# Performance work log

Measured on AMD Instinct MI355X. Metric: run time of the kernel, lower is better.

The kernel has to match this reference:

```python
import jax, jax.numpy as jnp
import numpy as np

B, DIM, T, H, MAX_T = 8, 512, 4096, 64, 4096


def setup_inputs() -> dict:
    key = jax.random.key(0)
    ks = jax.random.split(key, 10)
    s = 0.02  # small init scale keeps exp() well-conditioned, like xavier init
    x = jax.random.normal(ks[0], (B, DIM, T), dtype=jnp.float32)
    wq = jax.random.normal(ks[1], (H, DIM), dtype=jnp.float32) * s
    bq = jnp.zeros((H,), dtype=jnp.float32)
    wk = jax.random.normal(ks[2], (H, DIM), dtype=jnp.float32) * s
    bk = jnp.zeros((H,), dtype=jnp.float32)
    wv = jax.random.normal(ks[3], (H, DIM), dtype=jnp.float32) * s
    bv = jnp.zeros((H,), dtype=jnp.float32)
    wp = jax.random.normal(ks[4], (DIM, H), dtype=jnp.float32) * s
    bp = jnp.zeros((DIM,), dtype=jnp.float32)
    # xavier_uniform on [MAX_T, MAX_T]: bound = sqrt(6/(MAX_T+MAX_T))
    bound = float(np.sqrt(6.0 / (MAX_T + MAX_T)))
    wbias = jax.random.uniform(ks[5], (MAX_T, MAX_T), dtype=jnp.float32,
                               minval=-bound, maxval=bound)
    return {"x": x, "wq": wq, "bq": bq, "wk": wk, "bk": bk,
            "wv": wv, "bv": bv, "wp": wp, "bp": bp, "wbias": wbias}


def reference(x, wq, bq, wk, bk, wv, bv, wp, bp, wbias):
    # x: [B, dim, T] -> [B, T, dim]
    xt = jnp.swapaxes(x, 1, 2)
    t = xt.shape[1]
    Q = xt @ wq.T + bq            # [B, T, H]
    K = xt @ wk.T + bk            # [B, T, H]
    V = xt @ wv.T + bv            # [B, T, H]
    ew = jnp.exp(wbias[:t, :t])   # [T, T]
    eK = jnp.exp(K)               # [B, T, H]
    num = jnp.einsum('ts,bsh->bth', ew, eK * V)  # exp(w) @ (exp(K)*V)
    den = jnp.einsum('ts,bsh->bth', ew, eK)      # exp(w) @ exp(K)
    Yt = jax.nn.sigmoid(Q) * (num / den)          # [B, T, H]
    out = Yt @ wp.T + bp                          # [B, T, dim]
    return (out, out)
```

## Files before the change

### kernel.cpp

```cpp
#include <hip/hip_runtime.h>
#include <hip/hip_bf16.h>

#define B_   8
#define DIM_ 512
#define T_   4096
#define H_   64
#define NC_  1024

typedef __attribute__((ext_vector_type(8))) short short8;
typedef __attribute__((ext_vector_type(4))) float f32x4;

__device__ __forceinline__ unsigned short f2bf(float x) {
    __hip_bfloat16 h = __float2bfloat16(x);
    return *reinterpret_cast<unsigned short*>(&h);
}
__device__ __forceinline__ float bf2f(unsigned short u) {
    __hip_bfloat16 h = *reinterpret_cast<__hip_bfloat16*>(&u);
    return __bfloat162float(h);
}
__device__ __forceinline__ void gload16(const void* g, void* l) {
    __builtin_amdgcn_global_load_lds(
        (const __attribute__((address_space(1))) unsigned int*)g,
        (__attribute__((address_space(3))) unsigned int*)l, 16, 0, 0);
}

__global__ __launch_bounds__(256) void ewb_kernel(
    const float* __restrict__ wb, unsigned short* __restrict__ Aexp)
{
    const int n4 = T_ * T_ / 4;
    int idx = blockIdx.x * blockDim.x + threadIdx.x;
    int stride = gridDim.x * blockDim.x;
    for (int i = idx; i < n4; i += stride) {
        float4 v = ((const float4*)wb)[i];
        ushort4 o;
        o.x = f2bf(__expf(v.x));
        o.y = f2bf(__expf(v.y));
        o.z = f2bf(__expf(v.z));
        o.w = f2bf(__expf(v.w));
        ((ushort4*)Aexp)[i] = o;
    }
}

__global__ __launch_bounds__(128) void wcat_kernel(
    const float* __restrict__ wq, const float* __restrict__ bq,
    const float* __restrict__ wk, const float* __restrict__ bk,
    const float* __restrict__ wv, const float* __restrict__ bv,
    unsigned short* __restrict__ Wcat, float* __restrict__ bcat)
{
    const int r = blockIdx.x;
    const int tid = threadIdx.x;
    const float* src = (r < 64) ? (wq + (size_t)r * DIM_)
                     : (r < 128) ? (wk + (size_t)(r - 64) * DIM_)
                                 : (wv + (size_t)(r - 128) * DIM_);
    const int d4 = tid * 4;
    float4 v = *(const float4*)&src[d4];
    ushort4 o;
    o.x = f2bf(v.x); o.y = f2bf(v.y); o.z = f2bf(v.z); o.w = f2bf(v.w);
    *(ushort4*)&Wcat[(size_t)r * DIM_ + d4] = o;
    if (tid == 0)
        bcat[r] = (r < 64) ? bq[r] : (r < 128) ? bk[r - 64] : bv[r - 128];
}

__global__ __launch_bounds__(256) void wpb_kernel(
    const float* __restrict__ wp, unsigned short* __restrict__ wpb)
{
    const int i = (blockIdx.x * 256 + threadIdx.x) * 4;
    float4 v = *(const float4*)&wp[i];
    ushort4 o;
    o.x = f2bf(v.x); o.y = f2bf(v.y); o.z = f2bf(v.z); o.w = f2bf(v.w);
    *(ushort4*)&wpb[i] = o;
}

__global__ __launch_bounds__(256) void xqkv_fused(
    const float* __restrict__ x, const unsigned short* __restrict__ Wcat,
    const float* __restrict__ bcat,
    unsigned short* __restrict__ Qb, unsigned short* __restrict__ SbT)
{
    __shared__ float xs[64 * 65];
    __shared__ unsigned short Bs[192 * 64];

    const int tid = threadIdx.x;
    const int t0 = blockIdx.x * 64;
    const int b  = blockIdx.y;
    const int wid = tid >> 6, lane = tid & 63;

    f32x4 acc[12];
    const f32x4 vzero = {0.f, 0.f, 0.f, 0.f};
#pragma unroll
    for (int f = 0; f < 12; f++) acc[f] = vzero;

    const int rs  = tid >> 3;
    const int ks8 = (tid & 7) * 8;
    const unsigned short* Bg = Wcat + (size_t)rs * DIM_ + ks8;

    const int xrow = tid >> 4;
    const int xt4  = (tid & 15) * 4;

    const int t_in = lane & 15;
    const int g    = lane >> 4;

    for (int d0 = 0; d0 < DIM_; d0 += 64) {
#pragma unroll
        for (int p = 0; p < 4; p++) {
            const int d = p * 16 + xrow;
            float4 v = *(const float4*)&x[((size_t)b * DIM_ + d0 + d) * T_ + t0 + xt4];
            *(float4*)&xs[d * 65 + xt4] = v;
        }
#pragma unroll
        for (int it = 0; it < 6; it++)
            gload16(Bg + (size_t)(it * 32) * DIM_ + d0, (void*)&Bs[(it * 256 + tid) * 8]);
        __syncthreads();

        const int row_a = wid * 16 + t_in;
#pragma unroll
        for (int kk = 0; kk < 2; kk++) {
            union { unsigned short s[8]; short8 v; } af;
#pragma unroll
            for (int j = 0; j < 8; j++)
                af.s[j] = f2bf(xs[(kk * 32 + g * 8 + j) * 65 + row_a]);
            const int kr = kk * 32 + g * 8;
#pragma unroll
            for (int fn = 0; fn < 12; fn++) {
                short8 bf = *(const short8*)&Bs[(fn * 16 + t_in) * 64 + kr];
                acc[fn] = __builtin_amdgcn_mfma_f32_16x16x32_bf16(af.v, bf, acc[fn], 0, 0, 0);
            }
        }
        __syncthreads();
    }

    const int cc = t_in;
    const int t_base = t0 + wid * 16 + g * 4;

#pragma unroll
    for (int fn = 0; fn < 4; fn++) {
        const int h = fn * 16 + cc;
        const float bb = bcat[h];
#pragma unroll
        for (int r = 0; r < 4; r++)
            Qb[((size_t)b * T_ + t_base + r) * H_ + h] = f2bf(acc[fn][r] + bb);
    }
#pragma unroll
    for (int f = 0; f < 4; f++) {
        const int h = f * 16 + cc;
        const float bK = bcat[64 + h];
        const float bV = bcat[128 + h];
        ushort4 pk, pe;
        float e0 = __expf(acc[4 + f][0] + bK), v0 = acc[8 + f][0] + bV;
        float e1 = __expf(acc[4 + f][1] + bK), v1 = acc[8 + f][1] + bV;
        float e2 = __expf(acc[4 + f][2] + bK), v2 = acc[8 + f][2] + bV;
        float e3 = __expf(acc[4 + f][3] + bK), v3 = acc[8 + f][3] + bV;
        pe.x = f2bf(e0); pe.y = f2bf(e1); pe.z = f2bf(e2); pe.w = f2bf(e3);
        pk.x = f2bf(e0 * v0); pk.y = f2bf(e1 * v1); pk.z = f2bf(e2 * v2); pk.w = f2bf(e3 * v3);
        *(ushort4*)&SbT[(size_t)(b * 64 + h) * T_ + t_base] = pk;
        *(ushort4*)&SbT[(size_t)(512 + b * 64 + h) * T_ + t_base] = pe;
    }
}

__global__ __launch_bounds__(256) void aft_gemm_mfma(
    const unsigned short* __restrict__ Aexp,
    const unsigned short* __restrict__ SbT,
    unsigned short* __restrict__ ND)
{
    __shared__ unsigned short As[128 * 64];
    __shared__ unsigned short Bs[128 * 64];

    const int tid = threadIdx.x;
    const int lin = blockIdx.x + (blockIdx.y << 3) + (blockIdx.z << 8);
    const int swz = ((lin & 7) << 6) + (lin >> 3);
    const int c0 = (swz & 7) * 128;
    const int t0 = ((swz >> 3) & 31) * 128;
    const int ks = swz >> 8;
    const int sbase = ks * (T_ / 2);

    const int wid = tid >> 6, lane = tid & 63;
    const int wm = wid >> 1, wn = wid & 1;

    f32x4 acc[4][4];
    const f32x4 vzero = {0.f, 0.f, 0.f, 0.f};
#pragma unroll
    for (int a = 0; a < 4; a++)
#pragma unroll
        for (int b2 = 0; b2 < 4; b2++) acc[a][b2] = vzero;

    const int rs  = tid >> 3;
    const int ks8 = (tid & 7) * 8;
    const unsigned short* Ag = Aexp + (size_t)(t0 + rs) * T_ + sbase + ks8;
    const unsigned short* Bg = SbT  + (size_t)(c0 + rs) * T_ + sbase + ks8;

    for (int s0 = 0; s0 < T_ / 2; s0 += 64) {
#pragma unroll
        for (int it = 0; it < 4; it++) {
            gload16(Ag + (size_t)(it * 32) * T_ + s0, (void*)&As[(it * 256 + tid) * 8]);
            gload16(Bg + (size_t)(it * 32) * T_ + s0, (void*)&Bs[(it * 256 + tid) * 8]);
        }
        __syncthreads();
        const int row_a = wm * 64 + (lane & 15);
        const int row_b = wn * 64 + (lane & 15);
#pragma unroll
        for (int kk = 0; kk < 2; kk++) {
            const int kr = kk * 32 + (lane >> 4) * 8;
            short8 af[4], bfr[4];
#pragma unroll
            for (int f = 0; f < 4; f++)
                af[f] = *(const short8*)&As[(row_a + f * 16) * 64 + kr];
#pragma unroll
            for (int f = 0; f < 4; f++)
                bfr[f] = *(const short8*)&Bs[(row_b + f * 16) * 64 + kr];
#pragma unroll
            for (int fm = 0; fm < 4; fm++)
#pragma unroll
                for (int fn = 0; fn < 4; fn++)
                    acc[fm][fn] = __builtin_amdgcn_mfma_f32_16x16x32_bf16(
                        af[fm], bfr[fn], acc[fm][fn], 0, 0, 0);
        }
        __syncthreads();
    }

    unsigned short* NDp = ND + (size_t)ks * T_ * NC_;
    const int r4 = (lane >> 4) * 4;
    const int cc = lane & 15;
#pragma unroll
    for (int fm = 0; fm < 4; fm++)
#pragma unroll
        for (int fn = 0; fn < 4; fn++)
#pragma unroll
            for (int r = 0; r < 4; r++) {
                const int t = t0 + wm * 64 + fm * 16 + r4 + r;
                const int c = c0 + wn * 64 + fn * 16 + cc;
                NDp[(size_t)t * NC_ + c] = f2bf(acc[fm][fn][r]);
            }
}

__global__ __launch_bounds__(256) void epilogue_mfma(
    const unsigned short* __restrict__ Qb, const unsigned short* __restrict__ ND,
    const unsigned short* __restrict__ wpb, const float* __restrict__ bp,
    float* __restrict__ out, int write_both)
{
    __shared__ unsigned short smem[36864];
    unsigned short* y_s  = smem;
    unsigned short* wp_s = smem + 4096;
    float* st = (float*)smem;

    const int tid  = threadIdx.x;
    const int t0   = blockIdx.x * 64;
    const int b    = blockIdx.y;
    const int wid  = tid >> 6, lane = tid & 63;
    const size_t SZ_COPY = (size_t)B_ * T_ * DIM_;

    {
        const int rs = tid >> 3;
        const int c8 = tid & 7;
#pragma unroll
        for (int p = 0; p < 16; p++) {
            const int row = p * 32 + rs;
            gload16(wpb + (size_t)row * 64 + ((c8 ^ (row & 7)) << 3),
                    (void*)&wp_s[((size_t)row * 8 + c8) * 8]);
        }
    }
    {
        const int t   = tid >> 2;
        const int h16 = (tid & 3) * 16;
        const unsigned short* ND1 = ND + (size_t)T_ * NC_;
        const size_t qoff = ((size_t)b * T_ + t0 + t) * H_ + h16;
        const size_t noff = (size_t)(t0 + t) * NC_ + b * 64 + h16;
        float yv[16];
#pragma unroll
        for (int u = 0; u < 16; u++) {
            float q   = bf2f(Qb[qoff + u]);
            float num = bf2f(ND[noff + u]) + bf2f(ND1[noff + u]);
            float den = bf2f(ND[noff + 512 + u]) + bf2f(ND1[noff + 512 + u]);
            yv[u] = (1.f / (1.f + __expf(-q))) * num / den;
        }
#pragma unroll
        for (int u = 0; u < 2; u++) {
            const int h8 = (tid & 3) * 2 + u;
            union { unsigned short s[8]; short8 v; } pk;
#pragma unroll
            for (int e = 0; e < 8; e++) pk.s[e] = f2bf(yv[u * 8 + e]);
            *(short8*)((char*)y_s + t * 128 + ((h8 ^ (t & 7)) << 4)) = pk.v;
        }
    }
    __syncthreads();

    f32x4 acc[32];
    const f32x4 vzero = {0.f, 0.f, 0.f, 0.f};
#pragma unroll
    for (int f = 0; f < 32; f++) acc[f] = vzero;

    const int ra = wid * 16 + (lane & 15);
    short8 af[2];
#pragma unroll
    for (int kk = 0; kk < 2; kk++)
        af[kk] = *(const short8*)((char*)y_s + ra * 128 +
                                  (((kk * 4 + (lane >> 4)) ^ (ra & 7)) << 4));
#pragma unroll
    for (int fn = 0; fn < 32; fn++) {
        const int rb = fn * 16 + (lane & 15);
#pragma unroll
        for (int kk = 0; kk < 2; kk++) {
            short8 bf = *(const short8*)((char*)wp_s + rb * 128 +
                                         (((kk * 4 + (lane >> 4)) ^ (rb & 7)) << 4));
            acc[fn] = __builtin_amdgcn_mfma_f32_16x16x32_bf16(af[kk], bf, acc[fn], 0, 0, 0);
        }
    }
    __syncthreads();

    const int g  = lane >> 4;
    const int cc = lane & 15;
    float4 bb01[2];
    bb01[0] = *(const float4*)&bp[lane * 4];
    bb01[1] = *(const float4*)&bp[256 + lane * 4];

#pragma unroll
    for (int ch = 0; ch < 2; ch++) {
        if (ch) __syncthreads();
#pragma unroll
        for (int f = 0; f < 16; f++)
#pragma unroll
            for (int r = 0; r < 4; r++)
                st[(wid * 16 + g * 4 + r) * 260 + f * 16 + cc] = acc[ch * 16 + f][r];
        __syncthreads();
        const float4 bb = bb01[ch];
#pragma unroll
        for (int it = 0; it < 16; it++) {
            const int row = it * 4 + wid;
            float4 v = *(const float4*)&st[row * 260 + lane * 4];
            float4 o = {v.x + bb.x, v.y + bb.y, v.z + bb.z, v.w + bb.w};
            const size_t obase = ((size_t)b * T_ + t0 + row) * DIM_ + ch * 256 + lane * 4;
            *(float4*)&out[obase] = o;
            if (write_both)
                *(float4*)&out[SZ_COPY + obase] = o;
        }
    }
}

__global__ void dup_kernel(const float4* __restrict__ src, float4* __restrict__ dst, int n4)
{
    int idx = blockIdx.x * blockDim.x + threadIdx.x;
    int stride = gridDim.x * blockDim.x;
    for (int k = idx; k < n4; k += stride) dst[k] = src[k];
}

extern "C" void kernel_launch(void* const* d_in, const int* in_sizes, int n_in,
                              void* d_out, int out_size, void* d_ws, size_t ws_size,
                              hipStream_t stream)
{
    const float* x     = (const float*)d_in[0];
    const float* wq    = (const float*)d_in[1];
    const float* bq    = (const float*)d_in[2];
    const float* wk    = (const float*)d_in[3];
    const float* bk    = (const float*)d_in[4];
    const float* wv    = (const float*)d_in[5];
    const float* bv    = (const float*)d_in[6];
    const float* wp    = (const float*)d_in[7];
    const float* bp    = (const float*)d_in[8];
    const float* wbias = (const float*)d_in[9];
    float* out = (float*)d_out;

    const size_t SZ_COPY = (size_t)B_ * T_ * DIM_;

    const size_t NEED = 63177472;
    char* R;
    int write_both;
    if (ws_size >= NEED) {
        R = (char*)d_ws;
        write_both = 1;
    } else {
        R = (char*)(out + SZ_COPY);
        write_both = 0;
    }
    unsigned short* Aexp  = (unsigned short*)R;
    unsigned short* NDbuf = (unsigned short*)(R + 33554432);
    unsigned short* SbT   = (unsigned short*)(R + 50331648);
    unsigned short* Qbuf  = (unsigned short*)(R + 58720256);
    unsigned short* Wcat  = (unsigned short*)(R + 62914560);
    unsigned short* wpb   = (unsigned short*)(R + 63111168);
    float*          bcat  = (float*)(R + 63176704);

    ewb_kernel<<<2048, 256, 0, stream>>>(wbias, Aexp);
    wcat_kernel<<<192, 128, 0, stream>>>(wq, bq, wk, bk, wv, bv, Wcat, bcat);
    wpb_kernel<<<32, 256, 0, stream>>>(wp, wpb);
    xqkv_fused<<<dim3(T_ / 64, B_), 256, 0, stream>>>(x, Wcat, bcat, Qbuf, SbT);
    aft_gemm_mfma<<<dim3(NC_ / 128, T_ / 128, 2), 256, 0, stream>>>(Aexp, SbT, NDbuf);
    epilogue_mfma<<<dim3(T_ / 64, B_), 256, 0, stream>>>(Qbuf, NDbuf, wpb, bp, out, write_both);
    if (!write_both)
        dup_kernel<<<2048, 256, 0, stream>>>((const float4*)out,
                                             (float4*)(out + SZ_COPY),
                                             (int)(SZ_COPY / 4));
}
```

Measured before the change: 149.9 us.

## Rewrite AFT GEMM with 256x256 tiles, 8-phase double-buffered pipeline and split-K 4

Replaces the 128x128 single-buffered GEMM with a 512-thread, 256x256-tile kernel that double-buffers LDS and interleaves global-to-LDS loads across four MFMA phases per K step. It uses XOR-swizzled LDS layout and setprio around the MFMA bursts. The split-K factor rises to 4 when workspace allows, with the epilogue summing a variable number of partials. The aim is to hide load latency and raise arithmetic intensity, at the cost of more partial-sum traffic and 128KB of LDS per block.

```diff
diff --git a/kernel.cpp b/kernel.cpp
--- a/kernel.cpp
+++ b/kernel.cpp
@@ -156,77 +156,139 @@
     }
 }
 
-__global__ __launch_bounds__(256) void aft_gemm_mfma(
+__global__ __launch_bounds__(512, 2) void aft_gemm_8ph(
     const unsigned short* __restrict__ Aexp,
     const unsigned short* __restrict__ SbT,
-    unsigned short* __restrict__ ND)
-{
-    __shared__ unsigned short As[128 * 64];
-    __shared__ unsigned short Bs[128 * 64];
-
-    const int tid = threadIdx.x;
-    const int lin = blockIdx.x + (blockIdx.y << 3) + (blockIdx.z << 8);
-    const int swz = ((lin & 7) << 6) + (lin >> 3);
-    const int c0 = (swz & 7) * 128;
-    const int t0 = ((swz >> 3) & 31) * 128;
-    const int ks = swz >> 8;
-    const int sbase = ks * (T_ / 2);
-
-    const int wid = tid >> 6, lane = tid & 63;
-    const int wm = wid >> 1, wn = wid & 1;
-
-    f32x4 acc[4][4];
+    unsigned short* __restrict__ ND, int SK)
+{
+    __shared__ unsigned short smem[65536];
+
+    const int tid  = threadIdx.x;
+    const int wid  = tid >> 6, lane = tid & 63;
+    const int wm   = wid >> 2, wn = wid & 3;
+    const int la   = lane & 15, lg = lane >> 4;
+
+    const int nwg = 64 * SK;
+    const int lin = blockIdx.x + blockIdx.y * 4 + blockIdx.z * 64;
+    const int cpx = nwg >> 3;
+    const int wg  = (lin & 7) * cpx + (lin >> 3);
+    const int c0  = (wg & 3) * 256;
+    const int t0  = ((wg >> 2) & 15) * 256;
+    const int ks  = wg >> 6;
+    const int Kblk  = T_ / SK;
+    const int sbase = ks * Kblk;
+    const int NT    = Kblk >> 6;
+
+    f32x4 acc[8][4];
     const f32x4 vzero = {0.f, 0.f, 0.f, 0.f};
 #pragma unroll
-    for (int a = 0; a < 4; a++)
-#pragma unroll
-        for (int b2 = 0; b2 < 4; b2++) acc[a][b2] = vzero;
-
-    const int rs  = tid >> 3;
-    const int ks8 = (tid & 7) * 8;
-    const unsigned short* Ag = Aexp + (size_t)(t0 + rs) * T_ + sbase + ks8;
-    const unsigned short* Bg = SbT  + (size_t)(c0 + rs) * T_ + sbase + ks8;
-
-    for (int s0 = 0; s0 < T_ / 2; s0 += 64) {
-#pragma unroll
-        for (int it = 0; it < 4; it++) {
-            gload16(Ag + (size_t)(it * 32) * T_ + s0, (void*)&As[(it * 256 + tid) * 8]);
-            gload16(Bg + (size_t)(it * 32) * T_ + s0, (void*)&Bs[(it * 256 + tid) * 8]);
-        }
-        __syncthreads();
-        const int row_a = wm * 64 + (lane & 15);
-        const int row_b = wn * 64 + (lane & 15);
-#pragma unroll
-        for (int kk = 0; kk < 2; kk++) {
-            const int kr = kk * 32 + (lane >> 4) * 8;
-            short8 af[4], bfr[4];
-#pragma unroll
-            for (int f = 0; f < 4; f++)
-                af[f] = *(const short8*)&As[(row_a + f * 16) * 64 + kr];
-#pragma unroll
-            for (int f = 0; f < 4; f++)
-                bfr[f] = *(const short8*)&Bs[(row_b + f * 16) * 64 + kr];
-#pragma unroll
-            for (int fm = 0; fm < 4; fm++)
-#pragma unroll
-                for (int fn = 0; fn < 4; fn++)
-                    acc[fm][fn] = __builtin_amdgcn_mfma_f32_16x16x32_bf16(
-                        af[fm], bfr[fn], acc[fm][fn], 0, 0, 0);
-        }
-        __syncthreads();
+    for (int i = 0; i < 8; i++)
+#pragma unroll
+        for (int j = 0; j < 4; j++) acc[i][j] = vzero;
+
+    const int lr8 = tid >> 3, c16 = tid & 7;
+
+    auto stA = [&](int q, int T, int p) {
+        const int tr = (lr8 < 32) ? (32 * q + lr8) : (96 + 32 * q + lr8);
+        const unsigned short* src = Aexp + (size_t)(t0 + tr) * T_
+                                  + sbase + T * 64 + ((c16 ^ (tr & 7)) * 8);
+        gload16(src, (void*)&smem[p * 32768 + tr * 64 + c16 * 8]);
+    };
+    auto stB = [&](int h, int j, int T, int p) {
+        const int tr = 128 * h + 64 * j + lr8;
+        const unsigned short* src = SbT + (size_t)(c0 + tr) * T_
+                                  + sbase + T * 64 + ((c16 ^ (tr & 7)) * 8);
+        gload16(src, (void*)&smem[p * 32768 + 16384 + tr * 64 + c16 * 8]);
+    };
+
+    stB(0, 0, 0, 0); stB(0, 1, 0, 0); stB(1, 0, 0, 0); stB(1, 1, 0, 0);
+    stA(0, 0, 0);    stA(1, 0, 0);    stA(2, 0, 0);    stA(3, 0, 0);
+    stB(0, 0, 1, 1); stB(0, 1, 1, 1); stB(1, 0, 1, 1); stB(1, 1, 1, 1);
+    stA(0, 1, 1);    stA(1, 1, 1);
+    asm volatile("s_waitcnt vmcnt(6)" ::: "memory");
+    __builtin_amdgcn_s_barrier();
+
+    for (int kt = 0; kt < NT; ++kt) {
+        const int p = kt & 1;
+        const unsigned short* Ab = smem + p * 32768;
+        const unsigned short* Bb = Ab + 16384;
+        short8 bfr[4][2];
+
+        {
+            short8 af[2][2];
+#pragma unroll
+            for (int i = 0; i < 2; ++i) {
+                const int row = 128 * wm + 16 * i + la;
+#pragma unroll
+                for (int kk = 0; kk < 2; ++kk)
+                    af[i][kk] = *(const short8*)&Ab[row * 64 + (((kk * 4 + lg) ^ (row & 7)) * 8)];
+            }
+#pragma unroll
+            for (int fn = 0; fn < 4; ++fn) {
+                const int row = 64 * wn + 16 * fn + la;
+#pragma unroll
+                for (int kk = 0; kk < 2; ++kk)
+                    bfr[fn][kk] = *(const short8*)&Bb[row * 64 + (((kk * 4 + lg) ^ (row & 7)) * 8)];
+            }
+            if (kt + 1 < NT) { stA(2, kt + 1, 1 - p); stA(3, kt + 1, 1 - p); }
+            __builtin_amdgcn_s_barrier();
+            asm volatile("s_waitcnt lgkmcnt(0)" ::: "memory");
+            __builtin_amdgcn_sched_barrier(0);
+            __builtin_amdgcn_s_setprio(1);
+#pragma unroll
+            for (int i = 0; i < 2; ++i)
+#pragma unroll
+                for (int fn = 0; fn < 4; ++fn)
+#pragma unroll
+                    for (int kk = 0; kk < 2; ++kk)
+                        acc[i][fn] = __builtin_amdgcn_mfma_f32_16x16x32_bf16(
+                            af[i][kk], bfr[fn][kk], acc[i][fn], 0, 0, 0);
+            __builtin_amdgcn_s_setprio(0);
+            __builtin_amdgcn_s_barrier();
+        }
+#pragma unroll
+        for (int q = 1; q < 4; ++q) {
+            short8 af[2][2];
+#pragma unroll
+            for (int i = 0; i < 2; ++i) {
+                const int row = 128 * wm + 16 * (2 * q + i) + la;
+#pragma unroll
+                for (int kk = 0; kk < 2; ++kk)
+                    af[i][kk] = *(const short8*)&Ab[row * 64 + (((kk * 4 + lg) ^ (row & 7)) * 8)];
+            }
+            if (kt + 2 < NT) {
+                if (q == 1)      { stB(0, 0, kt + 2, p); stB(0, 1, kt + 2, p); }
+                else if (q == 2) { stB(1, 0, kt + 2, p); stB(1, 1, kt + 2, p); }
+                else             { stA(0, kt + 2, p);    stA(1, kt + 2, p);    }
+            }
+            if (q == 3) asm volatile("s_waitcnt vmcnt(6)" ::: "memory");
+            __builtin_amdgcn_s_barrier();
+            asm volatile("s_waitcnt lgkmcnt(0)" ::: "memory");
+            __builtin_amdgcn_sched_barrier(0);
+            __builtin_amdgcn_s_setprio(1);
+#pragma unroll
+            for (int i = 0; i < 2; ++i)
+#pragma unroll
+                for (int fn = 0; fn < 4; ++fn)
+#pragma unroll
+                    for (int kk = 0; kk < 2; ++kk)
+                        acc[2 * q + i][fn] = __builtin_amdgcn_mfma_f32_16x16x32_bf16(
+                            af[i][kk], bfr[fn][kk], acc[2 * q + i][fn], 0, 0, 0);
+            __builtin_amdgcn_s_setprio(0);
+            __builtin_amdgcn_s_barrier();
+        }
     }
 
     unsigned short* NDp = ND + (size_t)ks * T_ * NC_;
-    const int r4 = (lane >> 4) * 4;
-    const int cc = lane & 15;
-#pragma unroll
-    for (int fm = 0; fm < 4; fm++)
-#pragma unroll
-        for (int fn = 0; fn < 4; fn++)
-#pragma unroll
-            for (int r = 0; r < 4; r++) {
-                const int t = t0 + wm * 64 + fm * 16 + r4 + r;
-                const int c = c0 + wn * 64 + fn * 16 + cc;
+    const int r4 = lg * 4;
+#pragma unroll
+    for (int fm = 0; fm < 8; ++fm)
+#pragma unroll
+        for (int fn = 0; fn < 4; ++fn)
+#pragma unroll
+            for (int r = 0; r < 4; ++r) {
+                const int t = t0 + 128 * wm + 16 * fm + r4 + r;
+                const int c = c0 + 64 * wn + 16 * fn + la;
                 NDp[(size_t)t * NC_ + c] = f2bf(acc[fm][fn][r]);
             }
 }
@@ -234,7 +296,7 @@
 __global__ __launch_bounds__(256) void epilogue_mfma(
     const unsigned short* __restrict__ Qb, const unsigned short* __restrict__ ND,
     const unsigned short* __restrict__ wpb, const float* __restrict__ bp,
-    float* __restrict__ out, int write_both)
+    float* __restrict__ out, int write_both, int SK)
 {
     __shared__ unsigned short smem[36864];
     unsigned short* y_s  = smem;
@@ -260,15 +322,18 @@
     {
         const int t   = tid >> 2;
         const int h16 = (tid & 3) * 16;
-        const unsigned short* ND1 = ND + (size_t)T_ * NC_;
         const size_t qoff = ((size_t)b * T_ + t0 + t) * H_ + h16;
         const size_t noff = (size_t)(t0 + t) * NC_ + b * 64 + h16;
         float yv[16];
 #pragma unroll
         for (int u = 0; u < 16; u++) {
-            float q   = bf2f(Qb[qoff + u]);
-            float num = bf2f(ND[noff + u]) + bf2f(ND1[noff + u]);
-            float den = bf2f(ND[noff + 512 + u]) + bf2f(ND1[noff + 512 + u]);
+            float num = 0.f, den = 0.f;
+            for (int pp = 0; pp < SK; ++pp) {
+                const unsigned short* NDp = ND + (size_t)pp * T_ * NC_;
+                num += bf2f(NDp[noff + u]);
+                den += bf2f(NDp[noff + 512 + u]);
+            }
+            float q = bf2f(Qb[qoff + u]);
             yv[u] = (1.f / (1.f + __expf(-q))) * num / den;
         }
 #pragma unroll
@@ -359,30 +424,33 @@
 
     const size_t SZ_COPY = (size_t)B_ * T_ * DIM_;
 
-    const size_t NEED = 63177472;
+    auto need = [](int SK) -> size_t {
+        return 33554432u + (size_t)SK * 8388608u + 8388608u + 4194304u
+             + 196608u + 65536u + 1024u;
+    };
+    int SK, write_both;
     char* R;
-    int write_both;
-    if (ws_size >= NEED) {
-        R = (char*)d_ws;
-        write_both = 1;
+    if (ws_size >= need(4)) {
+        SK = 4; write_both = 1; R = (char*)d_ws;
     } else {
-        R = (char*)(out + SZ_COPY);
-        write_both = 0;
-    }
-    unsigned short* Aexp  = (unsigned short*)R;
-    unsigned short* NDbuf = (unsigned short*)(R + 33554432);
-    unsigned short* SbT   = (unsigned short*)(R + 50331648);
-    unsigned short* Qbuf  = (unsigned short*)(R + 58720256);
-    unsigned short* Wcat  = (unsigned short*)(R + 62914560);
-    unsigned short* wpb   = (unsigned short*)(R + 63111168);
-    float*          bcat  = (float*)(R + 63176704);
+        SK = 2; write_both = 0; R = (char*)(out + SZ_COPY);
+    }
+    size_t off = 0;
+    unsigned short* Aexp  = (unsigned short*)(R + off); off += 33554432u;
+    unsigned short* NDbuf = (unsigned short*)(R + off); off += (size_t)SK * 8388608u;
+    unsigned short* SbT   = (unsigned short*)(R + off); off += 8388608u;
+    unsigned short* Qbuf  = (unsigned short*)(R + off); off += 4194304u;
+    unsigned short* Wcat  = (unsigned short*)(R + off); off += 196608u;
+    unsigned short* wpb   = (unsigned short*)(R + off); off += 65536u;
+    float*          bcat  = (float*)(R + off);
 
     ewb_kernel<<<2048, 256, 0, stream>>>(wbias, Aexp);
     wcat_kernel<<<192, 128, 0, stream>>>(wq, bq, wk, bk, wv, bv, Wcat, bcat);
     wpb_kernel<<<32, 256, 0, stream>>>(wp, wpb);
     xqkv_fused<<<dim3(T_ / 64, B_), 256, 0, stream>>>(x, Wcat, bcat, Qbuf, SbT);
-    aft_gemm_mfma<<<dim3(NC_ / 128, T_ / 128, 2), 256, 0, stream>>>(Aexp, SbT, NDbuf);
-    epilogue_mfma<<<dim3(T_ / 64, B_), 256, 0, stream>>>(Qbuf, NDbuf, wpb, bp, out, write_both);
+    aft_gemm_8ph<<<dim3(4, 16, SK), 512, 0, stream>>>(Aexp, SbT, NDbuf, SK);
+    epilogue_mfma<<<dim3(T_ / 64, B_), 256, 0, stream>>>(Qbuf, NDbuf, wpb, bp, out,
+                                                         write_both, SK);
     if (!write_both)
         dup_kernel<<<2048, 256, 0, stream>>>((const float4*)out,
                                              (float4*)(out + SZ_COPY),
```

Result: slower. 184.8 us (+23.3%).
